# Optimization experiments

Measured on AMD Instinct MI355X. Metric: run time of the kernel, lower is better.

## Reference

```python
import jax, jax.numpy as jnp
import numpy as np

C = 512
NC = 12
EPS = 1e-5

ADJ = np.array([
    [0,0,0,1,0,1,1,1,1,1,1,1],
    [0,0,0,1,0,1,1,1,1,1,1,1],
    [0,0,0,1,0,1,1,1,1,1,1,1],
    [1,1,1,0,1,1,1,1,1,1,1,1],
    [0,0,0,1,0,1,1,1,1,1,1,1],
    [1,1,1,1,1,0,1,1,1,0,0,0],
    [1,1,1,1,1,1,0,0,0,1,1,1],
    [1,1,1,1,1,1,0,0,0,1,1,1],
    [1,1,1,1,1,1,0,0,0,1,1,1],
    [1,1,1,1,1,0,1,1,1,0,0,0],
    [1,1,1,1,1,0,1,1,1,0,0,0],
    [1,1,1,1,1,0,1,1,1,0,0,0]], dtype=np.float32)
# per-AU region selection: 0=up,1=mid,2=down1,3=down2 (AU1,2,4 up; AU6 mid; AU7 up; AU10 d2; AU12,14,15 d1; AU17,23,24 d2)
SEL = np.array([0,0,0,1,0,3,2,2,2,3,3,3])


def setup_inputs() -> dict:
    key = jax.random.key(0)
    ks = jax.random.split(key, 12)
    B, T = 32, 32
    BT = B * T
    s = (2.0 / C) ** 0.5
    return {
        'x': jax.random.normal(ks[0], (BT, 49, C), jnp.float32),
        'adj_mask': jnp.ones((BT, NC, NC), jnp.float32),
        'region_W': jax.random.normal(ks[1], (4, C, C), jnp.float32) * s,
        'region_b': jnp.zeros((4, C), jnp.float32),
        'region_gamma': jnp.ones((4, C), jnp.float32),
        'region_beta': jnp.zeros((4, C), jnp.float32),
        'upfc_W': jax.random.normal(ks[2], (C, 16), jnp.float32) * 0.02,
        'upfc_b': jnp.zeros((16,), jnp.float32),
        'midfc_W': jax.random.normal(ks[3], (C, 2), jnp.float32) * 0.02,
        'midfc_b': jnp.zeros((2,), jnp.float32),
        'd1fc_W': jax.random.normal(ks[4], (C, 8), jnp.float32) * 0.02,
        'd1fc_b': jnp.zeros((8,), jnp.float32),
        'd2fc_W': jax.random.normal(ks[5], (C, 16), jnp.float32) * 0.02,
        'd2fc_b': jnp.zeros((16,), jnp.float32),
        'class_W': jax.random.normal(ks[6], (NC, C, C), jnp.float32) * s,
        'class_b': jnp.zeros((NC, C), jnp.float32),
        'class_gamma': jnp.ones((NC, C), jnp.float32),
        'class_beta': jnp.zeros((NC, C), jnp.float32),
        'gat_W': jax.random.normal(ks[7], (C, C), jnp.float32) * 0.02,
        'gat_al': jax.random.normal(ks[8], (C,), jnp.float32) * 0.02,
        'gat_ar': jax.random.normal(ks[9], (C,), jnp.float32) * 0.02,
        'tconv_W': jax.random.normal(ks[10], (NC, C, 5), jnp.float32) * 0.1,
        'tconv_b': jnp.zeros((NC, C), jnp.float32),
        'tbn_gamma': jnp.ones((NC,), jnp.float32),
        'tbn_beta': jnp.zeros((NC,), jnp.float32),
        'B': B,
        'T': T,
    }


def _bn(x, gamma, beta, axes):
    # training-mode batch norm: stats over `axes`, affine per remaining channel
    mean = x.mean(axes, keepdims=True)
    var = x.var(axes, keepdims=True)
    return gamma * (x - mean) * jax.lax.rsqrt(var + EPS) + beta


def reference(x, adj_mask, region_W, region_b, region_gamma, region_beta,
              upfc_W, upfc_b, midfc_W, midfc_b, d1fc_W, d1fc_b, d2fc_W, d2fc_b,
              class_W, class_b, class_gamma, class_beta,
              gat_W, gat_al, gat_ar, tconv_W, tconv_b, tbn_gamma, tbn_beta, B, T):
    BT = x.shape[0]
    xg = x.reshape(BT, 7, 7, C)
    x_up = xg[:, :3].reshape(BT, 21, C)
    x_mid = xg[:, 2:5].reshape(BT, 21, C)
    x_down = xg[:, 4:].reshape(BT, 21, C)
    # 4 region LinearBlocks (fc -> BN over (batch,seq) per channel -> relu), batched
    regions = jnp.stack([x_up, x_mid, x_down, x_down])  # [4,BT,21,C]
    h = jnp.einsum('rbsc,rcd->rbsd', regions, region_W) + region_b[:, None, None, :]
    h = jax.nn.relu(_bn(h, region_gamma[:, None, None, :], region_beta[:, None, None, :], (1, 2)))
    up_pred = h[0].mean(1) @ upfc_W + upfc_b
    mid_pred = h[1].mean(1) @ midfc_W + midfc_b
    d1_pred = h[2].mean(1) @ d1fc_W + d1fc_b
    d2_pred = h[3].mean(1) @ d2fc_W + d2fc_b
    # 12 per-AU LinearBlocks, batched over the class dim
    cls_in = h[jnp.asarray(SEL)]  # [12,BT,21,C]
    y = jnp.einsum('nbsc,ncd->nbsd', cls_in, class_W) + class_b[:, None, None, :]
    y = jax.nn.relu(_bn(y, class_gamma[:, None, None, :], class_beta[:, None, None, :], (1, 2)))
    f_v = y.mean(2).transpose(1, 0, 2)  # [BT,12,C]
    # cross-region single-head GAT over the fixed 12-node graph, residual, thred=0.1
    adj = jnp.asarray(ADJ)[None] * adj_mask + jnp.eye(NC, dtype=x.dtype)
    hg = f_v @ gat_W  # [BT,12,C]
    e = jax.nn.leaky_relu((hg @ gat_al)[:, :, None] + (hg @ gat_ar)[:, None, :], 0.2)
    attn = jax.nn.softmax(jnp.where(adj > 0.1, e, -1e9), axis=-1)
    g = jnp.einsum('bij,bjc->bic', attn, hg) + f_v
    # per-class depthwise temporal Conv1d (k=5, pad=2, groups=C), batched over classes
    x4 = g.reshape(B, T, NC, C)
    xp = jnp.pad(x4, ((0, 0), (2, 2), (0, 0), (0, 0)))
    v = sum(xp[:, k:k + T] * tconv_W[None, None, :, :, k] for k in range(5)) + tconv_b[None, None]
    v = v.reshape(BT, NC, C)
    out = jax.nn.relu(_bn(v, tbn_gamma[None, :, None], tbn_beta[None, :, None], (0, 2)))
    return (up_pred, mid_pred, d1_pred, d2_pred, out)
```

## Files before the change

### kernel.cpp

```cpp
#include <hip/hip_runtime.h>
#include <hip/hip_bf16.h>

typedef unsigned short u16;
typedef __attribute__((ext_vector_type(8))) __bf16 bf16x8;
typedef __attribute__((ext_vector_type(8))) u16 u16x8;
typedef __attribute__((ext_vector_type(4))) u16 u16x4;
typedef __attribute__((ext_vector_type(4))) float floatx4;

#define C_     512
#define NC_    12
#define BT_    1024
#define SEQ_   21
#define M_REG  21504
#define M_GAT  12288

__device__ __forceinline__ float bf2f(u16 u) {
  unsigned int v = ((unsigned int)u) << 16;
  float f; __builtin_memcpy(&f, &v, 4); return f;
}
__device__ __forceinline__ u16 f2bf(float f) {
  unsigned int b; __builtin_memcpy(&b, &f, 4);
  unsigned int r = (b + 0x7FFFu + ((b >> 16) & 1u)) >> 16;
  return (u16)r;
}
__device__ __forceinline__ float ldf(const void* p, size_t i, int f32) {
  return f32 ? ((const float*)p)[i] : bf2f(((const u16*)p)[i]);
}
__device__ __forceinline__ u16 ldbf(const void* p, size_t i, int f32) {
  return f32 ? f2bf(((const float*)p)[i]) : ((const u16*)p)[i];
}
__device__ __forceinline__ void stout(void* p, size_t i, float v, int f32) {
  if (f32) ((float*)p)[i] = v; else ((u16*)p)[i] = f2bf(v);
}

typedef __attribute__((address_space(1))) unsigned int as1_u32;
typedef __attribute__((address_space(3))) unsigned int as3_u32;
__device__ __forceinline__ void gl2lds16(const void* g, void* l) {
  __builtin_amdgcn_global_load_lds((const as1_u32*)g, (as3_u32*)l, 16, 0, 0);
}

__global__ void sent_k(float* __restrict__ o, float val) {
  const int i = blockIdx.x * 256 + threadIdx.x;
  if (i < 16384) o[i] = val;
}

__global__ void detect_k(const u16* __restrict__ x, int* __restrict__ flag,
                         float* __restrict__ stats, int nstat) {
  if (blockIdx.x == 0) {
    __shared__ int cnt;
    if (threadIdx.x == 0) cnt = 0;
    __syncthreads();
    int bad = 0;
    for (int i = threadIdx.x; i < 4096; i += 256) {
      const float v = bf2f(x[i]);
      const float a = fabsf(v);
      if (!(a <= 1e4f)) bad++;
      else if (a > 0.f && a < 1e-35f) bad++;
    }
    atomicAdd(&cnt, bad);
    __syncthreads();
    if (threadIdx.x == 0) *flag = (cnt > 400) ? 1 : 0;
  } else {
    const int id = (blockIdx.x - 1) * 256 + threadIdx.x;
    if (id < nstat) stats[id] = 0.f;
  }
}

__global__ void transpose512(const void* __restrict__ rW, const void* __restrict__ cW,
                             const void* __restrict__ gW, u16* __restrict__ oR,
                             u16* __restrict__ oC, u16* __restrict__ oG,
                             const int* __restrict__ flagp) {
  const int f32 = *flagp;
  const int z = blockIdx.z;
  const void* src; u16* dst; size_t sofs = 0;
  if (z < 4)       { src = rW; sofs = (size_t)z*262144;     dst = oR + (size_t)z*262144; }
  else if (z < 16) { src = cW; sofs = (size_t)(z-4)*262144; dst = oC + (size_t)(z-4)*262144; }
  else             { src = gW;                              dst = oG; }
  __shared__ u16 t[32][33];
  const int tx = threadIdx.x;
  const int cy = blockIdx.y * 32, dx = blockIdx.x * 32;
  for (int i = threadIdx.y; i < 32; i += 8)
    t[i][tx] = ldbf(src, sofs + (size_t)(cy + i)*512 + dx + tx, f32);
  __syncthreads();
  for (int i = threadIdx.y; i < 32; i += 8)
    dst[(size_t)(dx + i)*512 + cy + tx] = t[tx][i];
}

template<int MODE>
__global__ __launch_bounds__(256)
void gemm_k(const void* __restrict__ Abase, const u16* __restrict__ Wtb,
            const void* __restrict__ biasb, u16* __restrict__ outb,
            float* __restrict__ ssumb, float* __restrict__ ssqb,
            const int* __restrict__ flagp, int pk, int n0)
{
  const int f32 = *flagp;
  const int z = blockIdx.z;
  const int zeff = (MODE == 1) ? (n0 + z) : z;
  const void* A = Abase;
  if (MODE == 1) A = (const void*)((const u16*)Abase +
        (size_t)((pk >> (zeff * 2)) & 3) * ((size_t)M_REG * C_));
  const u16* Wt = Wtb + (size_t)zeff * C_ * C_;
  u16* Out = outb + (size_t)z * (size_t)M_REG * C_;

  __shared__ __align__(16) u16 smem[64 * 132];
  u16* As = smem;
  u16* Bs = smem + 4096;

  const int tid  = threadIdx.x;
  const int w    = tid >> 6;
  const int lane = tid & 63;
  const int wm   = w >> 1, wn = w & 1;
  const int r16  = lane & 15, q = lane >> 4;

  const int band = (MODE == 2) ? 12 : 21;
  const int lin  = blockIdx.x;
  const int xcd  = lin & 7;
  const int idx  = lin >> 3;
  const int mi   = xcd * band + idx % band;
  const int ni   = idx / band;
  const int m0   = mi * 128;
  const int nn0  = ni * 128;

  const int sub = lane >> 2;
  const int kq  = (lane & 3) * 8;
  const int am0 = m0 + w*32 + sub;
  const int am1 = am0 + 16;
  long ga0, ga1;
  if (MODE == 0) {
    const int roff = (pk >> (z * 8)) & 0xFF;
    int q21 = am0 / 21; int rm = am0 - q21*21;
    ga0 = (long)q21*49 + roff + rm;
    q21 = am1 / 21; rm = am1 - q21*21;
    ga1 = (long)q21*49 + roff + rm;
  } else { ga0 = am0; ga1 = am1; }
  const size_t aOff0 = (size_t)ga0 * C_ + kq;
  const size_t aOff1 = (size_t)ga1 * C_ + kq;
  const u16* bSrc0 = Wt + (size_t)(nn0 + w*32 + sub) * C_ + kq;
  const u16* bSrc1 = bSrc0 + (size_t)16 * C_;
  u16* aDstW0 = &As[(w*32 +  0) * 32];
  u16* aDstW1 = &As[(w*32 + 16) * 32];
  u16* bDstW0 = &Bs[(w*32 +  0) * 32];
  u16* bDstW1 = &Bs[(w*32 + 16) * 32];
  u16x8* aLds0 = (u16x8*)&As[(w*32 + sub +  0) * 32 + kq];
  u16x8* aLds1 = (u16x8*)&As[(w*32 + sub + 16) * 32 + kq];

  floatx4 acc[4][4];
  #pragma unroll
  for (int i = 0; i < 4; i++)
    #pragma unroll
    for (int j = 0; j < 4; j++)
      acc[i][j] = (floatx4){0.f, 0.f, 0.f, 0.f};

  for (int kk = 0; kk < C_; kk += 32) {
    if (MODE == 0 && f32) {
      const float* p0 = (const float*)A + aOff0 + kk;
      const float* p1 = (const float*)A + aOff1 + kk;
      const floatx4 f00 = *(const floatx4*)p0;
      const floatx4 f01 = *(const floatx4*)(p0 + 4);
      const floatx4 f10 = *(const floatx4*)p1;
      const floatx4 f11 = *(const floatx4*)(p1 + 4);
      u16x8 va0, va1;
      #pragma unroll
      for (int j = 0; j < 4; j++) {
        va0[j] = f2bf(f00[j]); va0[4+j] = f2bf(f01[j]);
        va1[j] = f2bf(f10[j]); va1[4+j] = f2bf(f11[j]);
      }
      __syncthreads();
      gl2lds16(bSrc0, bDstW0); gl2lds16(bSrc1, bDstW1);
      *aLds0 = va0; *aLds1 = va1;
      __syncthreads();
    } else {
      __syncthreads();
      gl2lds16((const u16*)A + aOff0 + kk, aDstW0);
      gl2lds16((const u16*)A + aOff1 + kk, aDstW1);
      gl2lds16(bSrc0, bDstW0);
      gl2lds16(bSrc1, bDstW1);
      __syncthreads();
    }
    bSrc0 += 32; bSrc1 += 32;
    bf16x8 av[4], bv[4];
    #pragma unroll
    for (int mt = 0; mt < 4; mt++)
      av[mt] = *(const bf16x8*)&As[(wm*64 + mt*16 + r16)*32 + q*8];
    #pragma unroll
    for (int nt = 0; nt < 4; nt++)
      bv[nt] = *(const bf16x8*)&Bs[(wn*64 + nt*16 + r16)*32 + q*8];
    #pragma unroll
    for (int mt = 0; mt < 4; mt++)
      #pragma unroll
      for (int nt = 0; nt < 4; nt++)
        acc[mt][nt] = __builtin_amdgcn_mfma_f32_16x16x32_bf16(av[mt], bv[nt], acc[mt][nt], 0, 0, 0);
  }

  #pragma unroll
  for (int rh = 0; rh < 2; rh++) {
    __syncthreads();
    if (wm == rh) {
      #pragma unroll
      for (int nt = 0; nt < 4; nt++) {
        const int lcol = wn*64 + nt*16 + r16;
        float bvv = 0.f;
        if (MODE != 2) bvv = ldf(biasb, (size_t)zeff * C_ + nn0 + lcol, f32);
        float s = 0.f, s2 = 0.f;
        #pragma unroll
        for (int mt = 0; mt < 4; mt++) {
          #pragma unroll
          for (int p = 0; p < 4; p++) {
            const float v = acc[mt][nt][p] + bvv;
            s += v; s2 += v*v;
            smem[(mt*16 + q*4 + p)*132 + lcol] = f2bf(v);
          }
        }
        if (MODE != 2) {
          s  += __shfl_xor(s, 16);  s  += __shfl_xor(s, 32);
          s2 += __shfl_xor(s2, 16); s2 += __shfl_xor(s2, 32);
          if (q == 0) {
            atomicAdd(&ssumb[(size_t)zeff * C_ + nn0 + lcol], s);
            atomicAdd(&ssqb [(size_t)zeff * C_ + nn0 + lcol], s2);
          }
        }
      }
    }
    __syncthreads();
    #pragma unroll
    for (int rr = 0; rr < 4; rr++) {
      const int rl = rr*16 + (tid >> 4);
      const int cc = (tid & 15) * 8;
      const u16x8 vv = *(const u16x8*)&smem[rl*132 + cc];
      u16x8* dst = (u16x8*)&Out[(size_t)(m0 + rh*64 + rl) * C_ + nn0 + cc];
      if (MODE == 1) __builtin_nontemporal_store(vv, dst);
      else           *dst = vv;
    }
  }
}

__global__ void bn_region(u16* __restrict__ h, float* __restrict__ hbar,
                          const void* __restrict__ gamma, const void* __restrict__ beta,
                          const float* __restrict__ rsum, const float* __restrict__ rsq,
                          const int* __restrict__ flagp) {
  const int f32 = *flagp;
  const int gid  = blockIdx.x;
  const int r    = gid >> 8;
  const int bt   = ((gid & 255) << 2) + (threadIdx.x >> 6);
  const int lane = threadIdx.x & 63;
  const int d0   = lane * 8;
  const int rd   = r*512 + d0;
  float sc[8], sh[8], accv[8];
  #pragma unroll
  for (int j = 0; j < 8; j++) {
    const float mean = rsum[rd+j] * (1.f/21504.f);
    const float var  = fmaxf(rsq[rd+j] * (1.f/21504.f) - mean*mean, 0.f);
    sc[j] = ldf(gamma, rd+j, f32) * rsqrtf(var + 1e-5f);
    sh[j] = ldf(beta,  rd+j, f32) - mean * sc[j];
    accv[j] = 0.f;
  }
  const size_t base = ((size_t)r * M_REG + (size_t)bt * SEQ_) * C_ + d0;
  #pragma unroll
  for (int s = 0; s < SEQ_; s++) {
    u16x8 vv = *(u16x8*)&h[base + (size_t)s*C_];
    #pragma unroll
    for (int j = 0; j < 8; j++) {
      float v = fmaxf(sc[j] * bf2f(vv[j]) + sh[j], 0.f);
      vv[j] = f2bf(v);
      accv[j] += v;
    }
    *(u16x8*)&h[base + (size_t)s*C_] = vv;
  }
  float* hb = &hbar[((size_t)r * BT_ + bt) * C_ + d0];
  #pragma unroll
  for (int j = 0; j < 8; j++) hb[j] = accv[j] * (1.f/21.f);
}

__global__ void preds_k(const float* __restrict__ hbar,
                        const void* __restrict__ upW,  const void* __restrict__ upB,
                        const void* __restrict__ midW, const void* __restrict__ midB,
                        const void* __restrict__ d1W,  const void* __restrict__ d1B,
                        const void* __restrict__ d2W,  const void* __restrict__ d2B,
                        void* __restrict__ dout, const int* __restrict__ flagp) {
  const int f32 = *flagp;
  const int bt = blockIdx.x;
  __shared__ float hl[4][512];
  for (int i = threadIdx.x; i < 2048; i += 256)
    hl[i >> 9][i & 511] = hbar[((size_t)(i >> 9) * BT_ + bt) * C_ + (i & 511)];
  __syncthreads();
  const int w = threadIdx.x >> 6, lane = threadIdx.x & 63;
  for (int j = w; j < 42; j += 4) {
    int r, wdt, col; const void *W, *Bv; size_t oofs;
    if (j < 16)      { r=0; W=upW;  Bv=upB;  wdt=16; col=j;    oofs = (size_t)bt*16 + col; }
    else if (j < 18) { r=1; W=midW; Bv=midB; wdt=2;  col=j-16; oofs = 16384 + (size_t)bt*2 + col; }
    else if (j < 26) { r=2; W=d1W;  Bv=d1B;  wdt=8;  col=j-18; oofs = 18432 + (size_t)bt*8 + col; }
    else             { r=3; W=d2W;  Bv=d2B;  wdt=16; col=j-26; oofs = 26624 + (size_t)bt*16 + col; }
    float acc = 0.f;
    #pragma unroll
    for (int e = 0; e < 8; e++) {
      const int d = lane*8 + e;
      acc += hl[r][d] * ldf(W, (size_t)d*wdt + col, f32);
    }
    #pragma unroll
    for (int off = 32; off; off >>= 1) acc += __shfl_xor(acc, off);
    if (lane == 0) stout(dout, oofs, acc + ldf(Bv, col, f32), f32);
  }
}

__global__ void bn_class_mean(const u16* __restrict__ ypre, u16* __restrict__ fv,
                              const void* __restrict__ gamma, const void* __restrict__ beta,
                              const float* __restrict__ csum, const float* __restrict__ csq,
                              const int* __restrict__ flagp, int n0) {
  const int f32 = *flagp;
  const int gid  = blockIdx.x;
  const int zz   = gid >> 8;
  const int bt   = ((gid & 255) << 2) + (threadIdx.x >> 6);
  const int lane = threadIdx.x & 63;
  const int d0   = lane * 8;
  const int n    = n0 + zz;
  const int nd   = n*512 + d0;
  float sc[8], sh[8], accv[8];
  #pragma unroll
  for (int j = 0; j < 8; j++) {
    const float mean = csum[nd+j] * (1.f/21504.f);
    const float var  = fmaxf(csq[nd+j] * (1.f/21504.f) - mean*mean, 0.f);
    sc[j] = ldf(gamma, nd+j, f32) * rsqrtf(var + 1e-5f);
    sh[j] = ldf(beta,  nd+j, f32) - mean * sc[j];
    accv[j] = 0.f;
  }
  const size_t base = ((size_t)zz * M_REG + (size_t)bt * SEQ_) * C_ + d0;
  #pragma unroll
  for (int s = 0; s < SEQ_; s++) {
    const u16x8 vv = *(const u16x8*)&ypre[base + (size_t)s*C_];
    #pragma unroll
    for (int j = 0; j < 8; j++)
      accv[j] += fmaxf(sc[j] * bf2f(vv[j]) + sh[j], 0.f);
  }
  u16x8 ov;
  #pragma unroll
  for (int j = 0; j < 8; j++) ov[j] = f2bf(accv[j] * (1.f/21.f));
  *(u16x8*)&fv[((size_t)bt * NC_ + n) * C_ + d0] = ov;
}

__global__ __launch_bounds__(256)
void gat_k(const u16* __restrict__ hg, const u16* __restrict__ fv,
           const void* __restrict__ al, const void* __restrict__ ar,
           const void* __restrict__ adj_mask, float* __restrict__ g,
           const int* __restrict__ flagp) {
  const int f32 = *flagp;
  const int bt = blockIdx.x;
  __shared__ float hl[12][512];
  __shared__ float alv[12], arv[12], attn[12][12];
  const u16* hgb = hg + (size_t)bt * NC_ * C_;
  for (int i = threadIdx.x * 8; i < 6144; i += 2048) {
    const u16x8 vv = *(const u16x8*)&hgb[i];
    const int ii = i >> 9, cc = i & 511;
    #pragma unroll
    for (int e = 0; e < 8; e++) hl[ii][cc + e] = bf2f(vv[e]);
  }
  __syncthreads();
  const int w = threadIdx.x >> 6, lane = threadIdx.x & 63;
  for (int i = w; i < 12; i += 4) {
    float pa = 0.f, pr = 0.f;
    #pragma unroll
    for (int jj = 0; jj < 8; jj++) {
      const int c = lane*8 + jj;
      const float hv = hl[i][c];
      pa += hv * ldf(al, c, f32);
      pr += hv * ldf(ar, c, f32);
    }
    #pragma unroll
    for (int off = 32; off; off >>= 1) { pa += __shfl_xor(pa, off); pr += __shfl_xor(pr, off); }
    if (lane == 0) { alv[i] = pa; arv[i] = pr; }
  }
  __syncthreads();
  if (threadIdx.x < 12) {
    const unsigned AM[12] = {0xFE8,0xFE8,0xFE8,0xFF7,0xFE8,0x1DF,
                             0xE3F,0xE3F,0xE3F,0x1DF,0x1DF,0x1DF};
    const int i = threadIdx.x;
    float row[12]; float mx = -1e30f;
    #pragma unroll
    for (int jx = 0; jx < 12; jx++) {
      const float maskv = ldf(adj_mask, (size_t)bt*144 + i*12 + jx, f32);
      const float adjv = (float)((AM[i] >> jx) & 1u) * maskv + (i == jx ? 1.f : 0.f);
      float e;
      if (adjv > 0.1f) {
        const float t = alv[i] + arv[jx];
        e = t > 0.f ? t : 0.2f * t;
      } else e = -1e9f;
      row[jx] = e; mx = fmaxf(mx, e);
    }
    float den = 0.f;
    #pragma unroll
    for (int jx = 0; jx < 12; jx++) { const float ex = __expf(row[jx] - mx); row[jx] = ex; den += ex; }
    const float inv = 1.f / den;
    #pragma unroll
    for (int jx = 0; jx < 12; jx++) attn[i][jx] = row[jx] * inv;
  }
  __syncthreads();
  const u16* fvb = fv + (size_t)bt * NC_ * C_;
  float* gb = g + (size_t)bt * NC_ * C_;
  for (int o = threadIdx.x; o < 6144; o += 256) {
    const int i = o >> 9, c = o & 511;
    float acc = bf2f(fvb[o]);
    #pragma unroll
    for (int jx = 0; jx < 12; jx++) acc += attn[i][jx] * hl[jx][c];
    gb[o] = acc;
  }
}

__global__ void tconv_k(float* __restrict__ g, const void* __restrict__ tw,
                        const void* __restrict__ tb, float* __restrict__ tsum,
                        float* __restrict__ tsq, const int* __restrict__ flagp) {
  const int f32 = *flagp;
  const int id = blockIdx.x * 256 + threadIdx.x;
  const int c = id & 511;
  const int n = (id >> 9) % 12;
  const int b = id / 6144;
  float wk[5];
  #pragma unroll
  for (int k = 0; k < 5; k++) wk[k] = ldf(tw, (size_t)(n*512 + c)*5 + k, f32);
  const float bias = ldf(tb, n*512 + c, f32);
  float xv[36];
  xv[0] = xv[1] = xv[34] = xv[35] = 0.f;
  const size_t base = ((size_t)b * 32 * NC_ + n) * C_ + c;
  #pragma unroll
  for (int t = 0; t < 32; t++) xv[t + 2] = g[base + (size_t)t * 6144];
  float s = 0.f, s2 = 0.f;
  float ov[32];
  #pragma unroll
  for (int t = 0; t < 32; t++) {
    float v = bias;
    #pragma unroll
    for (int k = 0; k < 5; k++) v += wk[k] * xv[t + k];
    ov[t] = v; s += v; s2 += v*v;
  }
  #pragma unroll
  for (int t = 0; t < 32; t++) g[base + (size_t)t * 6144] = ov[t];
  #pragma unroll
  for (int off = 32; off; off >>= 1) { s += __shfl_xor(s, off); s2 += __shfl_xor(s2, off); }
  if ((threadIdx.x & 63) == 0) { atomicAdd(&tsum[n], s); atomicAdd(&tsq[n], s2); }
}

__global__ void bn_t(const float* __restrict__ v, void* __restrict__ outp,
                     const void* __restrict__ tg, const void* __restrict__ tb2,
                     const float* __restrict__ tsum, const float* __restrict__ tsq,
                     const int* __restrict__ flagp) {
  const int f32 = *flagp;
  const size_t id4 = (size_t)blockIdx.x * 256 + threadIdx.x;
  const int n = (int)((id4 >> 7) % 12);
  const float mean = tsum[n] * (1.f/524288.f);
  const float var  = fmaxf(tsq[n] * (1.f/524288.f) - mean*mean, 0.f);
  const float sc = ldf(tg, n, f32) * rsqrtf(var + 1e-5f);
  const float sh = ldf(tb2, n, f32) - mean * sc;
  const floatx4 vv = *(const floatx4*)&v[id4 * 4];
  if (f32) {
    floatx4 ov;
    #pragma unroll
    for (int e = 0; e < 4; e++) ov[e] = fmaxf(sc * vv[e] + sh, 0.f);
    *(floatx4*)&((float*)outp)[43008 + id4*4] = ov;
  } else {
    u16x4 ov;
    #pragma unroll
    for (int e = 0; e < 4; e++) ov[e] = f2bf(fmaxf(sc * vv[e] + sh, 0.f));
    *(u16x4*)&((u16*)outp)[43008 + id4*4] = ov;
  }
}

static constexpr size_t OFF_FLAG = 0;
static constexpr size_t OFF_STAT = 64;
static constexpr int    STAT_N   = 2048+2048+6144+6144+12+12;
static constexpr size_t OFF_WTR  = 65792;
static constexpr size_t OFF_WTC  = OFF_WTR + (size_t)4*512*512*2;
static constexpr size_t OFF_WTG  = OFF_WTC + (size_t)12*512*512*2;
static constexpr size_t OFF_H    = OFF_WTG + (size_t)512*512*2;
static constexpr size_t OFF_HBAR = OFF_H + (size_t)4*M_REG*C_*2;
static constexpr size_t OFF_FV   = OFF_HBAR + (size_t)4*BT_*C_*4;
static constexpr size_t OFF_AREN = OFF_FV + (size_t)M_GAT*C_*2;
static constexpr size_t YPRE_B   = (size_t)M_REG * C_ * 2;
static constexpr size_t NEEDED   = OFF_AREN + YPRE_B;

extern "C" void kernel_launch(void* const* d_in, const int* in_sizes, int n_in,
                              void* d_out, int out_size, void* d_ws, size_t ws_size,
                              hipStream_t stream) {
  const u16* x        = (const u16*)d_in[0];
  const void* adj_m   = d_in[1];
  const void* region_W= d_in[2];
  const void* region_b= d_in[3];
  const void* region_g= d_in[4];
  const void* region_be=d_in[5];
  const void* upW  = d_in[6];   const void* upB  = d_in[7];
  const void* midW = d_in[8];   const void* midB = d_in[9];
  const void* d1W  = d_in[10];  const void* d1B  = d_in[11];
  const void* d2W  = d_in[12];  const void* d2B  = d_in[13];
  const void* class_W = d_in[14];
  const void* class_b = d_in[15];
  const void* class_g = d_in[16];
  const void* class_be= d_in[17];
  const void* gat_W   = d_in[18];
  const void* gat_al  = d_in[19];
  const void* gat_ar  = d_in[20];
  const void* tconv_W = d_in[21];
  const void* tconv_b = d_in[22];
  const void* tbn_g   = d_in[23];
  const void* tbn_be  = d_in[24];

  char* ws = (char*)d_ws;
  int*   flagp = (int*)(ws + OFF_FLAG);
  float* rsum = (float*)(ws + OFF_STAT);
  float* rsq  = rsum + 2048;
  float* csum = rsq  + 2048;
  float* csq  = csum + 6144;
  float* tsum = csq  + 6144;
  float* tsq  = tsum + 12;
  u16*   WtR  = (u16*)(ws + OFF_WTR);
  u16*   WtC  = (u16*)(ws + OFF_WTC);
  u16*   WtG  = (u16*)(ws + OFF_WTG);
  u16*   h    = (u16*)(ws + OFF_H);
  float* hbar = (float*)(ws + OFF_HBAR);
  u16*   fv   = (u16*)(ws + OFF_FV);
  u16*   ypre = (u16*)(ws + OFF_AREN);
  u16*   hg   = (u16*)(ws + OFF_AREN);
  float* g    = (float*)(ws + OFF_H);

  int errStage = 0, errCode = 0;
  (void)hipGetLastError();
  #define CK(s) do { hipError_t e_ = hipGetLastError(); \
      if (e_ != hipSuccess && errStage == 0) { errStage = (s); errCode = (int)e_; } } while(0)

  sent_k<<<64, 256, 0, stream>>>((float*)d_out, 50.f); CK(12);

  if (ws_size < NEEDED) {
    int mb = (int)(ws_size >> 20); if (mb > 999) mb = 999;
    sent_k<<<64, 256, 0, stream>>>((float*)d_out, 13000.f + (float)mb);
    return;
  }

  int nch = (int)((ws_size - OFF_AREN) / YPRE_B);
  if (nch > 12) nch = 12;
  if (nch < 1) nch = 1;

  const int ROFFPACK = 0 | (14 << 8) | (28 << 16) | (28 << 24);
  const int SELPACK  = (1 << 6) | (3 << 10) | (2 << 12) | (2 << 14) |
                       (2 << 16) | (3 << 18) | (3 << 20) | (3 << 22);

  detect_k<<<1 + (STAT_N + 255)/256, 256, 0, stream>>>(x, flagp, rsum, STAT_N); CK(1);
  transpose512<<<dim3(16,16,17), dim3(32,8), 0, stream>>>(
      region_W, class_W, gat_W, WtR, WtC, WtG, flagp);               CK(2);

  gemm_k<0><<<dim3(672,1,4), 256, 0, stream>>>(
      x, WtR, region_b, h, rsum, rsq, flagp, ROFFPACK, 0);           CK(3);
  bn_region<<<1024, 256, 0, stream>>>(h, hbar, region_g, region_be,
      rsum, rsq, flagp);                                             CK(4);
  preds_k<<<1024, 256, 0, stream>>>(hbar, upW,upB, midW,midB,
      d1W,d1B, d2W,d2B, d_out, flagp);                               CK(5);

  for (int n0 = 0; n0 < 12; n0 += nch) {
    const int zc = (12 - n0) < nch ? (12 - n0) : nch;
    gemm_k<1><<<dim3(672,1,zc), 256, 0, stream>>>(
        h, WtC, class_b, ypre, csum, csq, flagp, SELPACK, n0);       CK(6);
    bn_class_mean<<<zc*256, 256, 0, stream>>>(ypre, fv, class_g, class_be,
        csum, csq, flagp, n0);                                       CK(7);
  }

  gemm_k<2><<<dim3(384,1,1), 256, 0, stream>>>(
      fv, WtG, nullptr, hg, nullptr, nullptr, flagp, 0, 0);          CK(8);
  gat_k<<<1024, 256, 0, stream>>>(hg, fv, gat_al, gat_ar, adj_m, g, flagp); CK(9);
  tconv_k<<<768, 256, 0, stream>>>(g, tconv_W, tconv_b, tsum, tsq, flagp);  CK(10);
  bn_t<<<6144, 256, 0, stream>>>(g, d_out, tbn_g, tbn_be, tsum, tsq, flagp); CK(11);

  if (errStage) {
    int ec = errCode > 999 ? 999 : errCode;
    sent_k<<<64, 256, 0, stream>>>((float*)d_out, (float)(errStage*1000 + ec));
  }
  #undef CK
}
```

Baseline: 786.2 us.

## Double GEMM K-tile to 64 and XOR-swizzle LDS layout

The GEMM kernel now loads a 64-wide K slice per iteration instead of 32, halving the number of barrier pairs per tile. It also stores A and B tiles in LDS with an XOR swizzle of 16-byte chunks by row, so the MFMA operand reads avoid bank conflicts. LDS use grows to 32 KB per block, which may reduce occupancy, and the swizzle has to match the direct global-to-LDS copy layout exactly.

```diff
diff --git a/kernel.cpp b/kernel.cpp
--- a/kernel.cpp
+++ b/kernel.cpp
@@ -102,15 +102,19 @@
   const u16* Wt = Wtb + (size_t)zeff * C_ * C_;
   u16* Out = outb + (size_t)z * (size_t)M_REG * C_;
 
-  __shared__ __align__(16) u16 smem[64 * 132];
+  __shared__ __align__(16) u16 smem[16384];
   u16* As = smem;
-  u16* Bs = smem + 4096;
+  u16* Bs = smem + 8192;
 
   const int tid  = threadIdx.x;
   const int w    = tid >> 6;
   const int lane = tid & 63;
   const int wm   = w >> 1, wn = w & 1;
   const int r16  = lane & 15, q = lane >> 4;
+
+  const int lr   = lane >> 3;
+  const int lc   = lane & 7;
+  const int csrc = lc ^ lr;
 
   const int band = (MODE == 2) ? 12 : 21;
   const int lin  = blockIdx.x;
@@ -121,28 +125,25 @@
   const int m0   = mi * 128;
   const int nn0  = ni * 128;
 
-  const int sub = lane >> 2;
-  const int kq  = (lane & 3) * 8;
-  const int am0 = m0 + w*32 + sub;
-  const int am1 = am0 + 16;
-  long ga0, ga1;
-  if (MODE == 0) {
-    const int roff = (pk >> (z * 8)) & 0xFF;
-    int q21 = am0 / 21; int rm = am0 - q21*21;
-    ga0 = (long)q21*49 + roff + rm;
-    q21 = am1 / 21; rm = am1 - q21*21;
-    ga1 = (long)q21*49 + roff + rm;
-  } else { ga0 = am0; ga1 = am1; }
-  const size_t aOff0 = (size_t)ga0 * C_ + kq;
-  const size_t aOff1 = (size_t)ga1 * C_ + kq;
-  const u16* bSrc0 = Wt + (size_t)(nn0 + w*32 + sub) * C_ + kq;
-  const u16* bSrc1 = bSrc0 + (size_t)16 * C_;
-  u16* aDstW0 = &As[(w*32 +  0) * 32];
-  u16* aDstW1 = &As[(w*32 + 16) * 32];
-  u16* bDstW0 = &Bs[(w*32 +  0) * 32];
-  u16* bDstW1 = &Bs[(w*32 + 16) * 32];
-  u16x8* aLds0 = (u16x8*)&As[(w*32 + sub +  0) * 32 + kq];
-  u16x8* aLds1 = (u16x8*)&As[(w*32 + sub + 16) * 32 + kq];
+  long gaA[4];
+  #pragma unroll
+  for (int j = 0; j < 4; j++) {
+    const int r = m0 + w*32 + j*8 + lr;
+    if (MODE == 0) {
+      const int roff = (pk >> (z * 8)) & 0xFF;
+      const int q21 = r / 21, rm = r - q21*21;
+      gaA[j] = (long)q21*49 + roff + rm;
+    } else gaA[j] = r;
+  }
+  const u16* aS[4]; const u16* bS[4];
+  u16* aD[4]; u16* bD[4];
+  #pragma unroll
+  for (int j = 0; j < 4; j++) {
+    aS[j] = (const u16*)A + (size_t)gaA[j] * C_ + csrc*8;
+    bS[j] = Wt + (size_t)(nn0 + w*32 + j*8 + lr) * C_ + csrc*8;
+    aD[j] = &As[(w*32 + j*8) * 64];
+    bD[j] = &Bs[(w*32 + j*8) * 64];
+  }
 
   floatx4 acc[4][4];
   #pragma unroll
@@ -151,45 +152,51 @@
     for (int j = 0; j < 4; j++)
       acc[i][j] = (floatx4){0.f, 0.f, 0.f, 0.f};
 
-  for (int kk = 0; kk < C_; kk += 32) {
+  for (int kk = 0; kk < C_; kk += 64) {
     if (MODE == 0 && f32) {
-      const float* p0 = (const float*)A + aOff0 + kk;
-      const float* p1 = (const float*)A + aOff1 + kk;
-      const floatx4 f00 = *(const floatx4*)p0;
-      const floatx4 f01 = *(const floatx4*)(p0 + 4);
-      const floatx4 f10 = *(const floatx4*)p1;
-      const floatx4 f11 = *(const floatx4*)(p1 + 4);
-      u16x8 va0, va1;
+      u16x8 va[4];
       #pragma unroll
       for (int j = 0; j < 4; j++) {
-        va0[j] = f2bf(f00[j]); va0[4+j] = f2bf(f01[j]);
-        va1[j] = f2bf(f10[j]); va1[4+j] = f2bf(f11[j]);
+        const float* p = (const float*)A + (size_t)gaA[j] * C_ + kk + lc*8;
+        const floatx4 f0 = *(const floatx4*)p;
+        const floatx4 f1 = *(const floatx4*)(p + 4);
+        #pragma unroll
+        for (int e = 0; e < 4; e++) { va[j][e] = f2bf(f0[e]); va[j][4+e] = f2bf(f1[e]); }
       }
       __syncthreads();
-      gl2lds16(bSrc0, bDstW0); gl2lds16(bSrc1, bDstW1);
-      *aLds0 = va0; *aLds1 = va1;
+      #pragma unroll
+      for (int j = 0; j < 4; j++) gl2lds16(bS[j], bD[j]);
+      #pragma unroll
+      for (int j = 0; j < 4; j++)
+        *(u16x8*)&As[(w*32 + j*8 + lr)*64 + ((lc ^ lr)*8)] = va[j];
       __syncthreads();
     } else {
       __syncthreads();
-      gl2lds16((const u16*)A + aOff0 + kk, aDstW0);
-      gl2lds16((const u16*)A + aOff1 + kk, aDstW1);
-      gl2lds16(bSrc0, bDstW0);
-      gl2lds16(bSrc1, bDstW1);
+      #pragma unroll
+      for (int j = 0; j < 4; j++) { gl2lds16(aS[j], aD[j]); gl2lds16(bS[j], bD[j]); }
       __syncthreads();
-    }
-    bSrc0 += 32; bSrc1 += 32;
-    bf16x8 av[4], bv[4];
-    #pragma unroll
-    for (int mt = 0; mt < 4; mt++)
-      av[mt] = *(const bf16x8*)&As[(wm*64 + mt*16 + r16)*32 + q*8];
-    #pragma unroll
-    for (int nt = 0; nt < 4; nt++)
-      bv[nt] = *(const bf16x8*)&Bs[(wn*64 + nt*16 + r16)*32 + q*8];
-    #pragma unroll
-    for (int mt = 0; mt < 4; mt++)
+      #pragma unroll
+      for (int j = 0; j < 4; j++) aS[j] += 64;
+    }
+    #pragma unroll
+    for (int j = 0; j < 4; j++) bS[j] += 64;
+
+    #pragma unroll
+    for (int s = 0; s < 2; s++) {
+      bf16x8 av[4], bv[4];
+      const int cs = (s*4 + q);
+      #pragma unroll
+      for (int mt = 0; mt < 4; mt++)
+        av[mt] = *(const bf16x8*)&As[(wm*64 + mt*16 + r16)*64 + ((cs ^ (r16 & 7))*8)];
       #pragma unroll
       for (int nt = 0; nt < 4; nt++)
-        acc[mt][nt] = __builtin_amdgcn_mfma_f32_16x16x32_bf16(av[mt], bv[nt], acc[mt][nt], 0, 0, 0);
+        bv[nt] = *(const bf16x8*)&Bs[(wn*64 + nt*16 + r16)*64 + ((cs ^ (r16 & 7))*8)];
+      #pragma unroll
+      for (int mt = 0; mt < 4; mt++)
+        #pragma unroll
+        for (int nt = 0; nt < 4; nt++)
+          acc[mt][nt] = __builtin_amdgcn_mfma_f32_16x16x32_bf16(av[mt], bv[nt], acc[mt][nt], 0, 0, 0);
+    }
   }
 
   #pragma unroll
```

Measured after the change: 825.5 us. 5.0% more time.
